# Kernel tuning notes

Hardware: AMD Instinct MI355X
Metric: run time of the kernel (lower is better)

## Reference

```python
import jax, jax.numpy as jnp
import numpy as np

LENS = 11          # odd aperture size (lens_mask init arg)
PAD = LENS // 2    # ReplicationPad2d(lens // 2)


def _distance_kernel(k):
    # k x k Euclidean distance from the kernel center
    c = k // 2
    ii, jj = np.meshgrid(np.arange(k), np.arange(k), indexing="ij")
    return np.sqrt((ii - c) ** 2 + (jj - c) ** 2).astype(np.float32)


def _lens_shape_mask(k):
    # circular aperture: 1 inside the disk of radius k//2
    return (_distance_kernel(k) <= k // 2).astype(np.float32)


def setup_inputs() -> dict:
    key = jax.random.key(0)
    kx, kl = jax.random.split(key)
    # RGBD input: channels 0..2 = color, channel 3 = relative disparity
    x = jax.random.normal(kx, (4, 4, 512, 512), dtype=jnp.float32)
    # per-image lens strength; scaled so splat radii span the full aperture
    lens_effects = jax.random.uniform(kl, (4, 1), dtype=jnp.float32) * 8.0
    return {
        "x": x,
        "lens_effects": lens_effects,
        "diskernel": jnp.asarray(_distance_kernel(LENS)),
        "lens_mask": jnp.asarray(_lens_shape_mask(LENS)),
    }


def _scatter_render(x, lens_effects, diskernel, lens_mask):
    """Depth-aware scatter (splat) bokeh blur.

    Each source pixel p splats its color onto every pixel within its circle of
    confusion radius r_p = clip(|disp_p| * lens_effect, 0, lens//2), with splat
    energy g_p = 1/(pi*r_p^2 + 1) (sharp pixels dominate).  Destinations
    normalize by the accumulated weight.  Implemented as the equivalent gather:
    out[q] = sum_o m_o * [r(q+o) >= d_o] * g(q+o) * rgb(q+o) / (same with rgb=1),
    scanning over the LENS*LENS offsets so no K^2-sized tensor is materialized.
    """
    B, C, H, W = x.shape
    rgb, disp = x[:, :3], x[:, 3:4]
    r = jnp.clip(jnp.abs(disp) * lens_effects[:, :, None, None], 0.0, float(PAD))
    g = 1.0 / (jnp.pi * r * r + 1.0)   # per-source splat energy (B,1,H,W)
    s = rgb * g                         # pre-scaled color (B,3,H,W)

    pad = ((0, 0), (0, 0), (PAD, PAD), (PAD, PAD))
    s_p = jnp.pad(s, pad, mode="edge")  # replication padding
    g_p = jnp.pad(g, pad, mode="edge")
    r_p = jnp.pad(r, pad, mode="edge")

    di = jnp.repeat(jnp.arange(LENS), LENS)
    dj = jnp.tile(jnp.arange(LENS), LENS)
    dists = diskernel.reshape(-1)
    masks = lens_mask.reshape(-1)

    def step(carry, inp):
        num, den = carry
        i, j, dist, mask = inp
        src_s = jax.lax.dynamic_slice(s_p, (0, 0, i, j), (B, 3, H, W))
        src_g = jax.lax.dynamic_slice(g_p, (0, 0, i, j), (B, 1, H, W))
        src_r = jax.lax.dynamic_slice(r_p, (0, 0, i, j), (B, 1, H, W))
        # coverage: source's circle of confusion reaches this destination
        cover = jax.lax.stop_gradient((src_r >= dist).astype(src_r.dtype))
        wm = mask * cover
        return (num + wm * src_s, den + wm * src_g), None

    init = (jnp.zeros((B, 3, H, W), x.dtype), jnp.zeros((B, 1, H, W), x.dtype))
    (num, den), _ = jax.lax.scan(step, init, (di, dj, dists, masks))
    # den > 0 always: the center offset (d=0, m=1) always covers itself
    return num / den


def reference(x, lens_effects, diskernel, lens_mask):
    return _scatter_render(x, lens_effects, diskernel, lens_mask)
```

## Files before the change

### kernel.cpp

```cpp
#include <hip/hip_runtime.h>

#define HH 512
#define WW 512
#define TILE 32
#define HALO 5
#define LT (TILE + 2 * HALO)
#define STR 43
#define PI_F 3.14159265358979323846f

constexpr int dimin(int dj) {
    return (dj == 0 || dj == 10) ? 5 : (dj == 1 || dj == 9) ? 2 : (dj == 5) ? 0 : 1;
}
constexpr int dimax(int dj) { return 10 - dimin(dj); }
constexpr int spv(int d2) {
    return d2 == 0 ? 0 : d2 == 1 ? 1 : d2 == 2 ? 2 : d2 == 4 ? 3 : d2 == 5 ? 4 :
           d2 == 8 ? 5 : d2 == 9 ? 6 : d2 == 10 ? 7 : d2 == 13 ? 8 : d2 == 16 ? 9 :
           d2 == 17 ? 10 : d2 == 18 ? 11 : d2 == 20 ? 12 : 13;
}

template <int DJ, int K, int P>
__device__ __forceinline__ void pstep(const float4& v, int rk, float (&acc)[4][4]) {
    constexpr int di = K - P;
    if constexpr (di >= dimin(DJ) && di <= dimax(DJ)) {
        constexpr int d2 = (di - 5) * (di - 5) + (DJ - 5) * (DJ - 5);
        const float wm = (rk > spv(d2)) ? 1.0f : 0.0f;
        acc[P][0] = fmaf(wm, v.x, acc[P][0]);
        acc[P][1] = fmaf(wm, v.y, acc[P][1]);
        acc[P][2] = fmaf(wm, v.z, acc[P][2]);
        acc[P][3] = fmaf(wm, v.w, acc[P][3]);
    }
}

template <int DJ, int K>
__device__ __forceinline__ void kstep(const float4* __restrict__ sgp, float (&acc)[4][4]) {
    if constexpr (K >= dimin(DJ) && K <= dimax(DJ) + 3) {
        const float4 v = sgp[K * STR + DJ];
        const int rk = (int)(__float_as_uint(v.w) & 15u);
        pstep<DJ, K, 0>(v, rk, acc);
        pstep<DJ, K, 1>(v, rk, acc);
        pstep<DJ, K, 2>(v, rk, acc);
        pstep<DJ, K, 3>(v, rk, acc);
    }
}

template <int DJ>
__device__ __forceinline__ void colstep(const float4* __restrict__ sgp, float (&acc)[4][4]) {
    kstep<DJ, 0>(sgp, acc);  kstep<DJ, 1>(sgp, acc);  kstep<DJ, 2>(sgp, acc);
    kstep<DJ, 3>(sgp, acc);  kstep<DJ, 4>(sgp, acc);  kstep<DJ, 5>(sgp, acc);
    kstep<DJ, 6>(sgp, acc);  kstep<DJ, 7>(sgp, acc);  kstep<DJ, 8>(sgp, acc);
    kstep<DJ, 9>(sgp, acc);  kstep<DJ, 10>(sgp, acc); kstep<DJ, 11>(sgp, acc);
    kstep<DJ, 12>(sgp, acc); kstep<DJ, 13>(sgp, acc);
}

__global__ __launch_bounds__(256, 4) void Scatter_Rendering_87101936763449_kernel(
    const float* __restrict__ x, const float* __restrict__ lens,
    const float* __restrict__ dk, float* __restrict__ out) {
    __shared__ float4 sg[LT * STR];

    const int b  = blockIdx.z;
    const int bx = blockIdx.x * TILE;
    const int by = blockIdx.y * TILE;
    const int t  = threadIdx.x;

    const float le = lens[b];
    const float* xb = x + (size_t)b * 4 * HH * WW;

    float dsort[14];
    {
        constexpr int AA[14] = {0, 0, 1, 0, 1, 2, 0, 1, 2, 0, 1, 3, 2, 0};
        constexpr int CC[14] = {0, 1, 1, 2, 2, 2, 3, 3, 3, 4, 4, 3, 4, 5};
#pragma unroll
        for (int k = 0; k < 14; ++k) dsort[k] = dk[(5 + AA[k]) * 11 + (5 + CC[k])];
    }

    for (int i = t; i < LT * LT; i += 256) {
        int ly = i / LT, lx = i - ly * LT;
        int gy = by + ly - HALO; gy = gy < 0 ? 0 : (gy > HH - 1 ? HH - 1 : gy);
        int gx = bx + lx - HALO; gx = gx < 0 ? 0 : (gx > WW - 1 ? WW - 1 : gx);
        int gi = gy * WW + gx;
        float d = xb[3 * HH * WW + gi];
        float r = fminf(fabsf(d) * le, (float)HALO);
        float g = 1.0f / (PI_F * r * r + 1.0f);
        int rank = 0;
#pragma unroll
        for (int k = 0; k < 14; ++k) rank += (r >= dsort[k]) ? 1 : 0;
        float gm = __uint_as_float((__float_as_uint(g) & ~15u) | (unsigned)rank);
        sg[ly * STR + lx] = make_float4(xb[gi] * g, xb[HH * WW + gi] * g,
                                        xb[2 * HH * WW + gi] * g, gm);
    }

    __syncthreads();

    const int tx   = t & 31;
    const int yloc = (t >> 5) * 4;

    float acc[4][4] = {{0.f}};
    const float4* sgp = &sg[yloc * STR + tx];

    colstep<0>(sgp, acc); colstep<1>(sgp, acc); colstep<2>(sgp, acc);
    colstep<3>(sgp, acc); colstep<4>(sgp, acc); colstep<5>(sgp, acc);
    colstep<6>(sgp, acc); colstep<7>(sgp, acc); colstep<8>(sgp, acc);
    colstep<9>(sgp, acc); colstep<10>(sgp, acc);

#pragma unroll
    for (int p = 0; p < 4; ++p) {
        const float inv = 1.0f / acc[p][3];
        const size_t o = (size_t)b * 3 * HH * WW + (size_t)(by + yloc + p) * WW + (bx + tx);
        out[o]               = acc[p][0] * inv;
        out[o + HH * WW]     = acc[p][1] * inv;
        out[o + 2 * HH * WW] = acc[p][2] * inv;
    }
}

extern "C" void kernel_launch(void* const* d_in, const int* in_sizes, int n_in,
                              void* d_out, int out_size, void* d_ws, size_t ws_size,
                              hipStream_t stream) {
    const float* x    = (const float*)d_in[0];
    const float* lens = (const float*)d_in[1];
    const float* dk   = (const float*)d_in[2];
    float* out = (float*)d_out;

    dim3 grid(WW / TILE, HH / TILE, 4);
    dim3 block(256);
    hipLaunchKernelGGL(Scatter_Rendering_87101936763449_kernel, grid, block, 0, stream,
                       x, lens, dk, out);
}
```

Before: 87.20 us.

## Compute 2x4 outputs per thread with even/odd column split shared tiles

Widens the tile to 64x32 so each thread computes two horizontally adjacent columns for four rows. Shared memory is split into even and odd column planes, so each loaded float4 feeds both output columns and LDS traffic per output drops. Output is written as float2 vector stores. The cost is more registers (occupancy hint lowered from 4 to 2 blocks) and a larger halo tile per block.

```diff
diff --git a/kernel.cpp b/kernel.cpp
--- a/kernel.cpp
+++ b/kernel.cpp
@@ -2,10 +2,12 @@
 
 #define HH 512
 #define WW 512
-#define TILE 32
+#define TX 64
+#define TY 32
 #define HALO 5
-#define LT (TILE + 2 * HALO)
-#define STR 43
+#define LTY (TY + 2 * HALO)
+#define NCP 37
+#define STRE 38
 #define PI_F 3.14159265358979323846f
 
 constexpr int dimin(int dj) {
@@ -17,49 +19,83 @@
            d2 == 8 ? 5 : d2 == 9 ? 6 : d2 == 10 ? 7 : d2 == 13 ? 8 : d2 == 16 ? 9 :
            d2 == 17 ? 10 : d2 == 18 ? 11 : d2 == 20 ? 12 : 13;
 }
+constexpr int rlo(int C) {
+    int lo = 100;
+    if (C <= 10) { int v = dimin(C);     if (v < lo) lo = v; }
+    if (C >= 1)  { int v = dimin(C - 1); if (v < lo) lo = v; }
+    return lo;
+}
+constexpr int rhi(int C) {
+    int hi = -100;
+    if (C <= 10) { int v = dimax(C) + 3;     if (v > hi) hi = v; }
+    if (C >= 1)  { int v = dimax(C - 1) + 3; if (v > hi) hi = v; }
+    return hi;
+}
 
-template <int DJ, int K, int P>
-__device__ __forceinline__ void pstep(const float4& v, int rk, float (&acc)[4][4]) {
-    constexpr int di = K - P;
-    if constexpr (di >= dimin(DJ) && di <= dimax(DJ)) {
-        constexpr int d2 = (di - 5) * (di - 5) + (DJ - 5) * (DJ - 5);
-        const float wm = (rk > spv(d2)) ? 1.0f : 0.0f;
-        acc[P][0] = fmaf(wm, v.x, acc[P][0]);
-        acc[P][1] = fmaf(wm, v.y, acc[P][1]);
-        acc[P][2] = fmaf(wm, v.z, acc[P][2]);
-        acc[P][3] = fmaf(wm, v.w, acc[P][3]);
+template <int C, int K, int S, int P>
+__device__ __forceinline__ void pstep(const float4& v, int rk, float (&acc)[2][4][4]) {
+    constexpr int dj = C - S;
+    if constexpr (dj >= 0 && dj <= 10) {
+        constexpr int di = K - P;
+        if constexpr (di >= dimin(dj) && di <= dimax(dj)) {
+            constexpr int d2 = (di - 5) * (di - 5) + (dj - 5) * (dj - 5);
+            const float wm = (rk > spv(d2)) ? 1.0f : 0.0f;
+            acc[S][P][0] = fmaf(wm, v.x, acc[S][P][0]);
+            acc[S][P][1] = fmaf(wm, v.y, acc[S][P][1]);
+            acc[S][P][2] = fmaf(wm, v.z, acc[S][P][2]);
+            acc[S][P][3] = fmaf(wm, v.w, acc[S][P][3]);
+        }
     }
 }
 
-template <int DJ, int K>
-__device__ __forceinline__ void kstep(const float4* __restrict__ sgp, float (&acc)[4][4]) {
-    if constexpr (K >= dimin(DJ) && K <= dimax(DJ) + 3) {
-        const float4 v = sgp[K * STR + DJ];
+template <int C, int K>
+__device__ __forceinline__ void kstep(const float4* __restrict__ eb,
+                                      const float4* __restrict__ ob,
+                                      float (&acc)[2][4][4]) {
+    if constexpr (K >= rlo(C) && K <= rhi(C)) {
+        const float4 v = (C & 1) ? ob[K * STRE + (C - 1) / 2] : eb[K * STRE + C / 2];
         const int rk = (int)(__float_as_uint(v.w) & 15u);
-        pstep<DJ, K, 0>(v, rk, acc);
-        pstep<DJ, K, 1>(v, rk, acc);
-        pstep<DJ, K, 2>(v, rk, acc);
-        pstep<DJ, K, 3>(v, rk, acc);
+        pstep<C, K, 0, 0>(v, rk, acc); pstep<C, K, 0, 1>(v, rk, acc);
+        pstep<C, K, 0, 2>(v, rk, acc); pstep<C, K, 0, 3>(v, rk, acc);
+        pstep<C, K, 1, 0>(v, rk, acc); pstep<C, K, 1, 1>(v, rk, acc);
+        pstep<C, K, 1, 2>(v, rk, acc); pstep<C, K, 1, 3>(v, rk, acc);
     }
 }
 
-template <int DJ>
-__device__ __forceinline__ void colstep(const float4* __restrict__ sgp, float (&acc)[4][4]) {
-    kstep<DJ, 0>(sgp, acc);  kstep<DJ, 1>(sgp, acc);  kstep<DJ, 2>(sgp, acc);
-    kstep<DJ, 3>(sgp, acc);  kstep<DJ, 4>(sgp, acc);  kstep<DJ, 5>(sgp, acc);
-    kstep<DJ, 6>(sgp, acc);  kstep<DJ, 7>(sgp, acc);  kstep<DJ, 8>(sgp, acc);
-    kstep<DJ, 9>(sgp, acc);  kstep<DJ, 10>(sgp, acc); kstep<DJ, 11>(sgp, acc);
-    kstep<DJ, 12>(sgp, acc); kstep<DJ, 13>(sgp, acc);
+template <int C>
+__device__ __forceinline__ void colstep(const float4* __restrict__ eb,
+                                        const float4* __restrict__ ob,
+                                        float (&acc)[2][4][4]) {
+    kstep<C, 0>(eb, ob, acc);  kstep<C, 1>(eb, ob, acc);  kstep<C, 2>(eb, ob, acc);
+    kstep<C, 3>(eb, ob, acc);  kstep<C, 4>(eb, ob, acc);  kstep<C, 5>(eb, ob, acc);
+    kstep<C, 6>(eb, ob, acc);  kstep<C, 7>(eb, ob, acc);  kstep<C, 8>(eb, ob, acc);
+    kstep<C, 9>(eb, ob, acc);  kstep<C, 10>(eb, ob, acc); kstep<C, 11>(eb, ob, acc);
+    kstep<C, 12>(eb, ob, acc); kstep<C, 13>(eb, ob, acc);
 }
 
-__global__ __launch_bounds__(256, 4) void Scatter_Rendering_87101936763449_kernel(
+__device__ __forceinline__ float4 mkpix(const float* __restrict__ xb,
+                                        const float (&dsort)[14], float le,
+                                        int gy, int gx) {
+    const int gi = gy * WW + gx;
+    const float d = xb[3 * HH * WW + gi];
+    const float r = fminf(fabsf(d) * le, (float)HALO);
+    const float g = 1.0f / (PI_F * r * r + 1.0f);
+    int rank = 0;
+#pragma unroll
+    for (int k = 0; k < 14; ++k) rank += (r >= dsort[k]) ? 1 : 0;
+    const float gm = __uint_as_float((__float_as_uint(g) & ~15u) | (unsigned)rank);
+    return make_float4(xb[gi] * g, xb[HH * WW + gi] * g, xb[2 * HH * WW + gi] * g, gm);
+}
+
+__global__ __launch_bounds__(256, 2) void Scatter_Rendering_87101936763449_kernel(
     const float* __restrict__ x, const float* __restrict__ lens,
     const float* __restrict__ dk, float* __restrict__ out) {
-    __shared__ float4 sg[LT * STR];
+    __shared__ float4 sgE[LTY * STRE];
+    __shared__ float4 sgO[LTY * STRE];
 
     const int b  = blockIdx.z;
-    const int bx = blockIdx.x * TILE;
-    const int by = blockIdx.y * TILE;
+    const int bx = blockIdx.x * TX;
+    const int by = blockIdx.y * TY;
     const int t  = threadIdx.x;
 
     const float le = lens[b];
@@ -73,42 +109,40 @@
         for (int k = 0; k < 14; ++k) dsort[k] = dk[(5 + AA[k]) * 11 + (5 + CC[k])];
     }
 
-    for (int i = t; i < LT * LT; i += 256) {
-        int ly = i / LT, lx = i - ly * LT;
+    for (int i = t; i < LTY * NCP; i += 256) {
+        const int ly = i / NCP, c = i - ly * NCP;
         int gy = by + ly - HALO; gy = gy < 0 ? 0 : (gy > HH - 1 ? HH - 1 : gy);
-        int gx = bx + lx - HALO; gx = gx < 0 ? 0 : (gx > WW - 1 ? WW - 1 : gx);
-        int gi = gy * WW + gx;
-        float d = xb[3 * HH * WW + gi];
-        float r = fminf(fabsf(d) * le, (float)HALO);
-        float g = 1.0f / (PI_F * r * r + 1.0f);
-        int rank = 0;
-#pragma unroll
-        for (int k = 0; k < 14; ++k) rank += (r >= dsort[k]) ? 1 : 0;
-        float gm = __uint_as_float((__float_as_uint(g) & ~15u) | (unsigned)rank);
-        sg[ly * STR + lx] = make_float4(xb[gi] * g, xb[HH * WW + gi] * g,
-                                        xb[2 * HH * WW + gi] * g, gm);
+        int ge = bx + 2 * c - HALO;     ge = ge < 0 ? 0 : (ge > WW - 1 ? WW - 1 : ge);
+        int go = bx + 2 * c - HALO + 1; go = go < 0 ? 0 : (go > WW - 1 ? WW - 1 : go);
+        sgE[ly * STRE + c] = mkpix(xb, dsort, le, gy, ge);
+        sgO[ly * STRE + c] = mkpix(xb, dsort, le, gy, go);
     }
 
     __syncthreads();
 
-    const int tx   = t & 31;
-    const int yloc = (t >> 5) * 4;
+    const int sx = t & 31;
+    const int sy = t >> 5;
+    const float4* eb = &sgE[(4 * sy) * STRE + sx];
+    const float4* ob = &sgO[(4 * sy) * STRE + sx];
 
-    float acc[4][4] = {{0.f}};
-    const float4* sgp = &sg[yloc * STR + tx];
+    float acc[2][4][4] = {{{0.f}}};
 
-    colstep<0>(sgp, acc); colstep<1>(sgp, acc); colstep<2>(sgp, acc);
-    colstep<3>(sgp, acc); colstep<4>(sgp, acc); colstep<5>(sgp, acc);
-    colstep<6>(sgp, acc); colstep<7>(sgp, acc); colstep<8>(sgp, acc);
-    colstep<9>(sgp, acc); colstep<10>(sgp, acc);
+    colstep<0>(eb, ob, acc); colstep<1>(eb, ob, acc); colstep<2>(eb, ob, acc);
+    colstep<3>(eb, ob, acc); colstep<4>(eb, ob, acc); colstep<5>(eb, ob, acc);
+    colstep<6>(eb, ob, acc); colstep<7>(eb, ob, acc); colstep<8>(eb, ob, acc);
+    colstep<9>(eb, ob, acc); colstep<10>(eb, ob, acc); colstep<11>(eb, ob, acc);
 
 #pragma unroll
     for (int p = 0; p < 4; ++p) {
-        const float inv = 1.0f / acc[p][3];
-        const size_t o = (size_t)b * 3 * HH * WW + (size_t)(by + yloc + p) * WW + (bx + tx);
-        out[o]               = acc[p][0] * inv;
-        out[o + HH * WW]     = acc[p][1] * inv;
-        out[o + 2 * HH * WW] = acc[p][2] * inv;
+        const float inv0 = 1.0f / acc[0][p][3];
+        const float inv1 = 1.0f / acc[1][p][3];
+        const int y = by + 4 * sy + p;
+#pragma unroll
+        for (int ch = 0; ch < 3; ++ch) {
+            float2 w = make_float2(acc[0][p][ch] * inv0, acc[1][p][ch] * inv1);
+            *reinterpret_cast<float2*>(
+                &out[((size_t)(b * 3 + ch) * HH + y) * WW + bx + 2 * sx]) = w;
+        }
     }
 }
 
@@ -120,7 +154,7 @@
     const float* dk   = (const float*)d_in[2];
     float* out = (float*)d_out;
 
-    dim3 grid(WW / TILE, HH / TILE, 4);
+    dim3 grid(WW / TX, HH / TY, 4);
     dim3 block(256);
     hipLaunchKernelGGL(Scatter_Rendering_87101936763449_kernel, grid, block, 0, stream,
                        x, lens, dk, out);
```

Measured after the change: 133.4 us. 1.53x slower.
